# Kernel optimization log

Measured on AMD Instinct MI355X. Metric: run time of the kernel, lower is better.

Reference implementation:

```python
import jax, jax.numpy as jnp
import numpy as np
from jax import lax

E, C, N = 3, 2, 2048          # edge types, channels, nodes (= nb_items)
B, T = 64, 50                 # batch, max_seq_length
W_IN = 256; W_OUT = 256; U = 512  # gcn in/out, rnn_units


def setup_inputs() -> dict:
    key = jax.random.key(0)
    ks = jax.random.split(key, 16)
    # sparse-ish adjacency stored densely (coalesce/spspmm equivalents are dense ops)
    A = jnp.where(jax.random.uniform(ks[0], (E, N, N)) < 0.01,
                  jax.random.uniform(ks[1], (E, N, N)), 0.0)
    X = jax.random.normal(ks[2], (N, W_IN)) * 0.1
    seqs = (jax.random.uniform(ks[3], (B, T, N)) < 0.005).astype(jnp.float32)  # multi-hot baskets
    seq_len = jax.random.randint(ks[4], (B,), 1, T + 1)
    h0 = jnp.zeros((B, U), jnp.float32)
    c0 = jnp.zeros((B, U), jnp.float32)
    # GTConv weights: init constant 1 (softmax -> uniform filter)
    gt_w1 = jnp.ones((C, E), jnp.float32)
    gt_w2 = jnp.ones((C, E), jnp.float32)
    gt_w3 = jnp.ones((C, E), jnp.float32)
    s_in = 1.0 / np.sqrt(W_IN)
    gcn_W = jax.random.normal(ks[5], (W_IN, W_OUT)) * s_in
    gcn_b = jnp.zeros((W_OUT,), jnp.float32)
    lin1_W = jax.random.normal(ks[6], (C * W_OUT, W_OUT)) * (1.0 / np.sqrt(C * W_OUT))
    lin1_b = jnp.zeros((W_OUT,), jnp.float32)
    s_u = 1.0 / np.sqrt(U)
    lstm_Wih = jax.random.normal(ks[7], (4 * U, W_OUT)) * s_u
    lstm_Whh = jax.random.normal(ks[8], (4 * U, U)) * s_u
    lstm_bih = jnp.zeros((4 * U,), jnp.float32)
    lstm_bhh = jnp.zeros((4 * U,), jnp.float32)
    score_W = jax.random.normal(ks[9], (N, U)) * s_u
    return {"A": A, "X": X, "seqs": seqs, "seq_len": seq_len, "h0": h0, "c0": c0,
            "gt_w1": gt_w1, "gt_w2": gt_w2, "gt_w3": gt_w3,
            "gcn_W": gcn_W, "gcn_b": gcn_b, "lin1_W": lin1_W, "lin1_b": lin1_b,
            "lstm_Wih": lstm_Wih, "lstm_Whh": lstm_Whh,
            "lstm_bih": lstm_bih, "lstm_bhh": lstm_bhh, "score_W": score_W}


def _gtconv(A, w):
    # filter = softmax over edge types; per-channel convex combine of adjacencies
    f = jax.nn.softmax(w, axis=1)            # [C,E]
    return jnp.einsum('ce,enm->cnm', f, A)   # [C,N,N]


def _col_normalize(H):
    # remove self loops; deg = scatter_add over col; value *= deg_col^-1 (no_grad deg)
    H = H * (1.0 - jnp.eye(N, dtype=H.dtype))
    deg = H.sum(axis=1)                      # [C,N] per-column degree
    dinv = lax.stop_gradient(jnp.where(deg > 0, 1.0 / deg, 0.0))
    return H * dinv[:, None, :]


def _gcn(M, X, W, b):
    # PyG GCNConv: add self loops, sym-normalize by col/row degree, aggregate at target
    M1 = M + jnp.eye(N, dtype=M.dtype)
    deg = M1.sum(axis=0)                     # scatter over col
    dis = jnp.where(deg > 0, lax.rsqrt(deg), 0.0)
    Ahat = dis[:, None] * M1 * dis[None, :]
    return Ahat.T @ (X @ W) + b              # out[target] = sum_src norm * x[src]


def reference(A, X, seqs, seq_len, h0, c0, gt_w1, gt_w2, gt_w3,
              gcn_W, gcn_b, lin1_W, lin1_b,
              lstm_Wih, lstm_Whh, lstm_bih, lstm_bhh, score_W):
    # --- GT layers: H = conv1(A) @ conv2(A), then H = norm(H) @ conv(A) ---
    HA = _gtconv(A, gt_w1)
    HB = _gtconv(A, gt_w2)
    H = jnp.einsum('cnk,ckm->cnm', HA, HB)          # spspmm per channel
    Hn = _col_normalize(H)
    HB2 = _gtconv(A, gt_w3)
    H = jnp.einsum('cnk,ckm->cnm', Hn, HB2)
    # --- GCN per channel, relu, concat, linear1 ---
    feats = [jax.nn.relu(_gcn(H[i], X, gcn_W, gcn_b)) for i in range(C)]
    X_ = jnp.concatenate(feats, axis=1) @ lin1_W + lin1_b   # [N, W_OUT]
    # --- basket max-pooling over items in each basket (empty -> zeros) ---
    def pool_step(_, mask_t):                # mask_t: [B,N]
        masked = jnp.where(mask_t[:, :, None] > 0, X_[None, :, :], -jnp.inf)
        pooled = masked.max(axis=1)          # [B, W_OUT]
        has = mask_t.sum(axis=1) > 0
        return None, jnp.where(has[:, None], pooled, 0.0)
    _, bs = lax.scan(pool_step, None, jnp.swapaxes(seqs, 0, 1))  # [T,B,W_OUT]
    # --- single-layer LSTM (PyTorch gate order i,f,g,o) ---
    def lstm_step(carry, x_t):
        h, c = carry
        g = x_t @ lstm_Wih.T + h @ lstm_Whh.T + lstm_bih + lstm_bhh
        i, f, gg, o = jnp.split(g, 4, axis=-1)
        c = jax.nn.sigmoid(f) * c + jax.nn.sigmoid(i) * jnp.tanh(gg)
        h = jax.nn.sigmoid(o) * jnp.tanh(c)
        return (h, c), h
    _, outs = lax.scan(lstm_step, (h0, c0), bs)      # [T,B,U]
    lstm_out = jnp.swapaxes(outs, 0, 1)              # [B,T,U]
    actual = lstm_out[jnp.arange(B), seq_len - 1]    # [B,U] last valid step
    return jax.nn.sigmoid(actual @ score_W.T)        # [B,N]
```

## Files before the change

kernel.cpp:

```cpp
#include <hip/hip_runtime.h>
#include <stdint.h>

#define E_ 3
#define C_ 2
#define N_ 2048
#define B_ 64
#define T_ 50
#define WIN_ 256
#define WOUT_ 256
#define U_ 512
#define BT_ (B_*T_)
#define BTP_ 3328

typedef unsigned short u16;
typedef unsigned int u32;
typedef __bf16 bf16x8 __attribute__((ext_vector_type(8)));
typedef float f32x4 __attribute__((ext_vector_type(4)));

#define NN_ (2048LL*2048LL)

__device__ __forceinline__ float bf2f(u16 u){
  u32 x = ((u32)u) << 16; return __builtin_bit_cast(float, x);
}
__device__ __forceinline__ u16 f2bf(float f){
  u32 x = __builtin_bit_cast(u32, f);
  u32 r = (x + 0x7fffu + ((x >> 16) & 1u)) >> 16;
  return (u16)r;
}

__device__ __forceinline__ void gload16(const u16* g, u16* l){
  __builtin_amdgcn_global_load_lds((const __attribute__((address_space(1))) u32*)g,
                                   (__attribute__((address_space(3))) u32*)l, 16, 0, 0);
}

__global__ void k_prep0(const float* __restrict__ w1, const float* __restrict__ w2,
                        const float* __restrict__ w3, float* __restrict__ filt,
                        const float* __restrict__ bih, const float* __restrict__ bhh,
                        float* __restrict__ bsum, u32* __restrict__ flagv,
                        const float* __restrict__ X, u16* __restrict__ Xbf,
                        const float* __restrict__ Wih, u16* __restrict__ Wihbf,
                        const float* __restrict__ scoreW, u16* __restrict__ sWbf){
  const long bx = blockIdx.x;
  if(bx < 8192){
    const long i = bx*256 + threadIdx.x;
    if(i < (long)N_*WIN_) Xbf[i] = f2bf(X[i]);
    else if(i < (long)N_*WIN_ + 4*U_*WOUT_){
      const long j = i - (long)N_*WIN_; Wihbf[j] = f2bf(Wih[j]);
    } else {
      const long j = i - (long)N_*WIN_ - 4*U_*WOUT_; sWbf[j] = f2bf(scoreW[j]);
    }
    return;
  }
  const int i = (int)(bx - 8192)*256 + threadIdx.x;
  bsum[i] = bih[i] + bhh[i];
  flagv[i] = 0;
  if(i < 3*C_){
    const int fi = i / C_, c = i % C_;
    const float* w = (fi==0) ? w1 : ((fi==1) ? w2 : w3);
    float v[E_]; float mx = -3.4e38f;
    for(int e=0;e<E_;e++){ v[e] = w[c*E_+e]; mx = fmaxf(mx, v[e]); }
    float s = 0.f;
    for(int e=0;e<E_;e++){ v[e] = expf(v[e]-mx); s += v[e]; }
    for(int e=0;e<E_;e++) filt[(fi*C_+c)*E_ + e] = v[e]/s;
  }
}

__global__ void k_combineAll3(const float* __restrict__ A, const float* __restrict__ filt,
                              u16* __restrict__ HA, u16* __restrict__ HBt,
                              u16* __restrict__ HB2t){
  __shared__ float te[3][32][33];
  const int ti = blockIdx.x, tj = blockIdx.y;
  const int x = threadIdx.x, y0 = threadIdx.y;
  #pragma unroll
  for(int i=0;i<4;i++){
    const int y = y0 + i*8;
    const long base = (long)(tj*32+y)*N_ + ti*32 + x;
    const float a0 = A[0*NN_+base], a1 = A[1*NN_+base], a2 = A[2*NN_+base];
    te[0][y][x]=a0; te[1][y][x]=a1; te[2][y][x]=a2;
    #pragma unroll
    for(int c=0;c<C_;c++)
      HA[c*NN_ + base] = f2bf(filt[c*E_]*a0 + filt[c*E_+1]*a1 + filt[c*E_+2]*a2);
  }
  __syncthreads();
  #pragma unroll
  for(int i=0;i<4;i++){
    const int y = y0 + i*8;
    const long ob = (long)(ti*32+y)*N_ + tj*32 + x;
    const float a0=te[0][x][y], a1=te[1][x][y], a2=te[2][x][y];
    #pragma unroll
    for(int c=0;c<C_;c++){
      HBt[c*NN_+ob]  = f2bf(filt[(C_+c)*E_]*a0   + filt[(C_+c)*E_+1]*a1   + filt[(C_+c)*E_+2]*a2);
      HB2t[c*NN_+ob] = f2bf(filt[(2*C_+c)*E_]*a0 + filt[(2*C_+c)*E_+1]*a1 + filt[(2*C_+c)*E_+2]*a2);
    }
  }
}

template<int MODE>
__global__ __launch_bounds__(256) void gemm_bt(
    const u16* __restrict__ Ag, const u16* __restrict__ Bg, void* __restrict__ Cg,
    int K, int ldc, long sA, long sB, long sC,
    const float* __restrict__ disv, int sDis, const float* __restrict__ bias)
{
  __shared__ u16 At[2][128*64];
  __shared__ u16 Bt[2][128*64];
  const int tid = threadIdx.x;
  const int w = tid >> 6, l = tid & 63;
  const int z = blockIdx.z;
  const int zc = (MODE==7) ? (z >> 2) : z;
  const int kBase = (MODE==7) ? ((z & 3)*sDis) : 0;
  const u16* Ab = Ag + (long)zc*sA;
  const u16* Bb = Bg + (long)z*sB;
  const int rowBase = blockIdx.y*128;
  const int colBase = blockIdx.x*128;

  f32x4 acc[4][4];
  #pragma unroll
  for(int i=0;i<4;i++)
    #pragma unroll
    for(int j=0;j<4;j++)
      acc[i][j] = f32x4{0.f,0.f,0.f,0.f};

  const int wr = w >> 1, wc = w & 1;
  const int srow = l >> 3;
  const int scol = ((l & 7) ^ srow) << 3;
  const int frow = l & 15;
  const int fkc = l >> 4;

  const int nk = (MODE==7) ? (sDis >> 6) : (K >> 6);
  #pragma unroll
  for(int r=0;r<4;r++){
    const int ch = w*4 + r;
    gload16(Ab + (long)(rowBase + ch*8 + srow)*K + kBase + scol, &At[0][ch*512]);
    gload16(Bb + (long)(colBase + ch*8 + srow)*K + kBase + scol, &Bt[0][ch*512]);
  }
  __syncthreads();

  for(int kt=0; kt<nk; ++kt){
    const int cur = kt & 1;
    if(kt+1 < nk){
      const int k0 = kBase + ((kt+1) << 6);
      #pragma unroll
      for(int r=0;r<4;r++){
        const int ch = w*4 + r;
        gload16(Ab + (long)(rowBase + ch*8 + srow)*K + k0 + scol, &At[cur^1][ch*512]);
        gload16(Bb + (long)(colBase + ch*8 + srow)*K + k0 + scol, &Bt[cur^1][ch*512]);
      }
    }
    #pragma unroll
    for(int ks=0; ks<2; ++ks){
      bf16x8 af[4], bfv[4];
      #pragma unroll
      for(int m=0;m<4;m++){
        const int rr = wr*64 + m*16 + frow;
        af[m] = *(const bf16x8*)&At[cur][rr*64 + (((ks*4 + fkc) ^ (rr&7))<<3)];
      }
      #pragma unroll
      for(int n=0;n<4;n++){
        const int rr = wc*64 + n*16 + frow;
        bfv[n] = *(const bf16x8*)&Bt[cur][rr*64 + (((ks*4 + fkc) ^ (rr&7))<<3)];
      }
      #pragma unroll
      for(int m=0;m<4;m++)
        #pragma unroll
        for(int n=0;n<4;n++)
          acc[m][n] = __builtin_amdgcn_mfma_f32_16x16x32_bf16(af[m], bfv[n], acc[m][n], 0, 0, 0);
    }
    if(kt+1 < nk) __syncthreads();
  }

  #pragma unroll
  for(int m=0;m<4;m++){
    const int row0 = rowBase + wr*64 + m*16 + (l>>4)*4;
    #pragma unroll
    for(int n=0;n<4;n++){
      const int col = colBase + wc*64 + n*16 + (l&15);
      #pragma unroll
      for(int r=0;r<4;r++){
        const float v = acc[m][n][r];
        if(MODE==1){
          ((u16*)Cg)[z*sC + (long)(row0+r)*ldc + col] = f2bf(v);
        } else if(MODE==2){
          float o = disv[z*(long)sDis + row0 + r]*v + bias[col];
          o = o > 0.f ? o : 0.f;
          ((u16*)Cg)[z*sC + (long)(row0+r)*ldc + col] = f2bf(o);
        } else if(MODE==3){
          ((float*)Cg)[z*sC + (long)(row0+r)*ldc + col] = v + bias[col];
        } else if(MODE==4){
          const int row = row0 + r;
          if(row < BT_){
            const int bb = row/50, tt = row - bb*50;
            const int gate = col >> 9, ugg = col & 511;
            ((float*)Cg)[((((long)tt*4 + (bb>>4))*512 + ugg)*16 + (bb&15))*4 + gate] = v + bias[col];
          }
        } else if(MODE==5){
          const int row = row0 + r;
          const float o = (v + (row==col ? 1.f : 0.f)) * disv[z*(long)sDis + col];
          ((u16*)Cg)[z*sC + (long)row*ldc + col] = f2bf(o);
        } else if(MODE==6){
          const int row = row0 + r;
          if(row < B_)
            ((float*)Cg)[(long)row*ldc + col] = 1.f/(1.f + expf(-v));
        } else if(MODE==7){
          ((float*)Cg)[((long)z*N_ + row0 + r)*WOUT_ + col] = v;
        }
      }
    }
  }
}

__global__ void k_catred(const float* __restrict__ P, const float* __restrict__ disv,
                         const float* __restrict__ gcnB, u16* __restrict__ catb){
  const int idx = blockIdx.x*256 + threadIdx.x;
  const int row = idx >> 9;
  const int cf  = idx & 511;
  const int c = cf >> 8, f = cf & 255;
  float s = 0.f;
  #pragma unroll
  for(int ks=0;ks<4;ks++)
    s += P[(((long)(c*4+ks)*N_ + row)<<8) + f];
  float o = disv[c*N_ + row]*s + gcnB[f];
  catb[(long)row*(C_*WOUT_) + cf] = f2bf(o > 0.f ? o : 0.f);
}

__global__ void k_degpart(const u16* __restrict__ H, float* __restrict__ partial){
  const int c = blockIdx.z;
  const int col = blockIdx.x*256 + threadIdx.x;
  const int r0 = blockIdx.y*128;
  const u16* Hc = H + c*NN_;
  float s = 0.f;
  #pragma unroll 4
  for(int r=0;r<128;r++) s += bf2f(Hc[(long)(r0+r)*N_ + col]);
  partial[((long)c*16 + blockIdx.y)*N_ + col] = s;
}

__global__ void k_dinv(const u16* __restrict__ H, const float* __restrict__ partial,
                       float* __restrict__ dinvb){
  const int i = blockIdx.x*256 + threadIdx.x;
  const int c = i >> 11, m = i & (N_-1);
  float s = 0.f;
  #pragma unroll
  for(int p=0;p<16;p++) s += partial[((long)c*16 + p)*N_ + m];
  s -= bf2f(H[c*NN_ + (long)m*N_ + m]);
  dinvb[i] = s > 0.f ? 1.f/s : 0.f;
}

__global__ void k_colscale_dis(u16* __restrict__ H, const float* __restrict__ dinvb,
                               const u16* __restrict__ HB2t, float* __restrict__ disv){
  const int c = blockIdx.y;
  if(blockIdx.x < 16384){
    const long i = (long)blockIdx.x*256 + threadIdx.x;
    const int j = (int)(i >> 11), ii = (int)(i & (N_-1));
    const long idx = c*NN_ + i;
    const float v = (j==ii) ? 0.f : bf2f(H[idx])*dinvb[c*N_ + ii];
    H[idx] = f2bf(v);
    return;
  }
  const int j = blockIdx.x - 16384;
  const u16* r = HB2t + (c*(long)N_ + j)*N_;
  const float* dv = dinvb + c*N_;
  float s = 0.f;
  for(int i=threadIdx.x;i<N_;i+=256)
    if(dv[i] > 0.f) s += bf2f(r[i]);
  __shared__ float red[256];
  red[threadIdx.x] = s;
  __syncthreads();
  for(int st=128; st>0; st>>=1){
    if(threadIdx.x < st) red[threadIdx.x] += red[threadIdx.x+st];
    __syncthreads();
  }
  if(threadIdx.x==0){
    const float deg = red[0] + 1.f;
    disv[c*N_ + j] = deg > 0.f ? rsqrtf(deg) : 0.f;
  }
}

__global__ void k_transpose3(const float* __restrict__ gcnW, u16* __restrict__ Wt,
                             const float* __restrict__ lin1W, u16* __restrict__ l1Wt){
  const float* in; u16* out; int R, Cc;
  if(blockIdx.z==0){ in=gcnW;  out=Wt;   R=WIN_;     Cc=WOUT_; }
  else { in=lin1W; out=l1Wt; R=C_*WOUT_; Cc=WOUT_; }
  const int ti = blockIdx.x, tj = blockIdx.y;
  if(ti >= (Cc>>5) || tj >= (R>>5)) return;
  __shared__ float tt[32][33];
  const int x = threadIdx.x, y0 = threadIdx.y;
  #pragma unroll
  for(int i=0;i<4;i++){
    const int y = y0 + i*8;
    tt[y][x] = in[(long)(tj*32+y)*Cc + ti*32 + x];
  }
  __syncthreads();
  #pragma unroll
  for(int i=0;i<4;i++){
    const int y = y0 + i*8;
    out[(long)(ti*32+y)*R + tj*32 + x] = f2bf(tt[x][y]);
  }
}

__global__ void k_pool(const float* __restrict__ seqs, const float* __restrict__ X_,
                       u16* __restrict__ bs){
  const int t = blockIdx.x, b = blockIdx.y;
  const int f = threadIdx.x;
  if(t >= T_){
    bs[(long)(BT_ + b*2 + (t-T_))*WOUT_ + f] = 0;
    return;
  }
  const float* mask = seqs + ((long)b*T_ + t)*N_;
  __shared__ int list[N_];
  __shared__ int cnt;
  if(f==0) cnt = 0;
  __syncthreads();
  {
    const float4 m0 = *(const float4*)&mask[f*8];
    const float4 m1 = *(const float4*)&mask[f*8+4];
    const float mv[8] = {m0.x,m0.y,m0.z,m0.w,m1.x,m1.y,m1.z,m1.w};
    #pragma unroll
    for(int q=0;q<8;q++){
      if(mv[q] > 0.f){
        int p = atomicAdd(&cnt, 1);
        list[p] = f*8 + q;
      }
    }
  }
  __syncthreads();
  const int m = cnt;
  float mx = -3.4e38f;
  for(int i=0;i<m;i++)
    mx = fmaxf(mx, X_[(long)list[i]*WOUT_ + f]);
  bs[((long)b*T_ + t)*WOUT_ + f] = f2bf(m>0 ? mx : 0.f);
}

__global__ void k_packWhh3(const float* __restrict__ Whh, u16* __restrict__ P,
                           const float* __restrict__ h0, u16* __restrict__ Hglob){
  const long idx = (long)blockIdx.x*256 + threadIdx.x;
  const int e  = (int)(idx & 7);
  const int kk = (int)((idx >> 3) & 15);
  const int l  = (int)((idx >> 7) & 63);
  const int w  = (int)((idx >> 13) & 7);
  const int s  = (int)(idx >> 16);
  const int lr = w*16 + (l & 15);
  const int gam = lr & 3, ui = lr >> 2;
  const int grow = gam*512 + s*32 + ui;
  const int k = kk*32 + (l >> 4)*8 + e;
  P[idx] = f2bf(Whh[(long)grow*512 + k]);
  if(idx < 32768){
    const int b = (int)(idx >> 9), u = (int)(idx & 511);
    const int grp = b >> 4, bl = b & 15;
    Hglob[grp*16384 + (bl << 9) + (u ^ ((bl & 7) << 3))] = f2bf(h0[idx]);
  }
}

__global__ __launch_bounds__(512) void k_lstm_all(
    const u16* __restrict__ WhhP, const float* __restrict__ Gq,
    const float* __restrict__ c0v, const int* __restrict__ seqlen,
    u16* __restrict__ Hglob, u32* __restrict__ flagv, u16* __restrict__ act)
{
  __shared__ u16 Hl[16*512];
  const int tid = threadIdx.x;
  const int w = tid >> 6, l = tid & 63;
  const int grp = blockIdx.x & 3, s = blockIdx.x >> 2;
  const int fr = l & 15, hi = l >> 4;

  bf16x8 wreg[16];
  const u16* wp = WhhP + (((long)s*8 + w)*64 + l)*128;
  #pragma unroll
  for(int kk=0; kk<16; ++kk)
    wreg[kk] = *(const bf16x8*)&wp[kk*8];

  const int ug = s*32 + w*4 + hi;
  const int bl = fr;
  const int bg = grp*16 + bl;
  float cst = c0v[bg*U_ + ug];
  const int sl = seqlen[bg] - 1;
  u16* Hbase = Hglob + grp*16384;
  const int hswz = (bl & 7) << 3;
  const int fi = (grp*16 + fr)*32;
  const long gqbase = (((long)grp*512 + ug)*16 + bl)*4;
  float4 gq_nxt = *(const float4*)&Gq[gqbase];

  for(int t=0; t<T_; ++t){
    const float4 gq = gq_nxt;
    const u16* Hin = Hbase + (t & 1)*8192;
    #pragma unroll
    for(int r=0; r<2; ++r)
      gload16(Hin + (r*8 + w)*512 + l*8, &Hl[(r*8 + w)*512]);
    __syncthreads();

    f32x4 acc = f32x4{0.f,0.f,0.f,0.f};
    #pragma unroll
    for(int kk=0; kk<16; ++kk){
      const int ke = kk*32 + hi*8;
      bf16x8 bb = *(const bf16x8*)&Hl[(bl << 9) + (ke ^ hswz)];
      acc = __builtin_amdgcn_mfma_f32_16x16x32_bf16(wreg[kk], bb, acc, 0, 0, 0);
    }

    if(t+1 < T_)
      gq_nxt = *(const float4*)&Gq[(long)(t+1)*(4*2048*16) + gqbase];

    const float a0 = acc[0] + gq.x;
    const float a1 = acc[1] + gq.y;
    const float a2 = acc[2] + gq.z;
    const float a3 = acc[3] + gq.w;
    const float ig = 1.f/(1.f + expf(-a0));
    const float fg = 1.f/(1.f + expf(-a1));
    const float gg = tanhf(a2);
    const float og = 1.f/(1.f + expf(-a3));
    cst = fg*cst + ig*gg;
    const float h = og*tanhf(cst);
    u16* Hout = Hbase + ((t+1) & 1)*8192;
    Hout[(bl << 9) + (ug ^ hswz)] = f2bf(h);
    if(sl == t) act[bg*U_ + ug] = f2bf(h);

    if(t == T_-1) break;
    __syncthreads();
    if(tid == 0)
      __hip_atomic_store(&flagv[(grp*16 + s)*32], (u32)(t+1),
                         __ATOMIC_RELEASE, __HIP_MEMORY_SCOPE_AGENT);
    if(w == 0){
      while(__hip_atomic_load(&flagv[fi], __ATOMIC_ACQUIRE,
                              __HIP_MEMORY_SCOPE_AGENT) <= (u32)t){
        __builtin_amdgcn_s_sleep(1);
      }
    }
    __syncthreads();
  }
}

extern "C" void kernel_launch(void* const* d_in, const int* in_sizes, int n_in,
                              void* d_out, int out_size, void* d_ws, size_t ws_size,
                              hipStream_t stream){
  (void)in_sizes; (void)n_in; (void)out_size; (void)ws_size;
  const float* A      = (const float*)d_in[0];
  const float* X      = (const float*)d_in[1];
  const float* seqs   = (const float*)d_in[2];
  const int*   seqlen = (const int*)d_in[3];
  const float* h0     = (const float*)d_in[4];
  const float* c0     = (const float*)d_in[5];
  const float* gtw1   = (const float*)d_in[6];
  const float* gtw2   = (const float*)d_in[7];
  const float* gtw3   = (const float*)d_in[8];
  const float* gcnW   = (const float*)d_in[9];
  const float* gcnB   = (const float*)d_in[10];
  const float* lin1W  = (const float*)d_in[11];
  const float* lin1B  = (const float*)d_in[12];
  const float* Wih    = (const float*)d_in[13];
  const float* Whh    = (const float*)d_in[14];
  const float* bihp   = (const float*)d_in[15];
  const float* bhhp   = (const float*)d_in[16];
  const float* scoreW = (const float*)d_in[17];

  char* ws = (char*)d_ws;
  u16* buf0 = (u16*)(ws + 0);
  u16* buf1 = (u16*)(ws + 16777216);
  u16* buf2 = (u16*)(ws + 33554432);
  char* S0  = ws + 50331648;
  float* filt  = (float*)(S0 + 0);
  float* disv  = (float*)(S0 + 1024);
  u16*  Wt     = (u16*) (S0 + 17408);
  u16*  XWt    = (u16*) (S0 + 148480);
  u16*  catb   = (u16*) (S0 + 1197056);
  u16*  l1Wt   = (u16*) (S0 + 3294208);
  float* Xo    = (float*)(S0 + 3556352);
  u16*  bs     = (u16*) (S0 + 5653504);
  u16*  act    = (u16*) (S0 + 7357440);
  u16*  sWbf   = (u16*) (S0 + 7488512);
  u16*  WhhB   = (u16*) (S0 + 9585664);
  u16*  Xbf    = (u16*) (S0 + 11682816);
  u16*  Wihbf  = (u16*) (S0 + 12731392);
  float* bsum  = (float*)(S0 + 13779968);
  u16*  Hglob  = (u16*) (S0 + 13788160);
  u32*  flagv  = (u32*) (S0 + 13919232);
  float* degp  = (float*)(S0 + 14050304);
  float* dinvb = (float*)(S0 + 14312448);
  u16* buf3 = (u16*)(ws + 64660480);
  u16* HA   = buf0;
  u16* HBt  = buf1;
  u16* Hb   = buf2;
  u16* HB2t = buf3;
  u16* Pd   = buf1;
  float* Pcat = (float*)ws;
  float* Gq = (float*)ws;

  k_prep0<<<dim3(8200), 256, 0, stream>>>(gtw1, gtw2, gtw3, filt, bihp, bhhp, bsum, flagv,
                                          X, Xbf, Wih, Wihbf, scoreW, sWbf);
  k_combineAll3<<<dim3(N_/32, N_/32), dim3(32,8), 0, stream>>>(A, filt, HA, HBt, HB2t);
  k_transpose3<<<dim3(16, 64, 2), dim3(32,8), 0, stream>>>(gcnW, Wt, lin1W, l1Wt);
  gemm_bt<1><<<dim3(16,16,C_), 256, 0, stream>>>(HA, HBt, Hb, N_, N_, NN_, NN_, NN_, nullptr, 0, nullptr);
  k_degpart<<<dim3(8, 16, C_), 256, 0, stream>>>(Hb, degp);
  k_dinv<<<dim3(16), 256, 0, stream>>>(Hb, degp, dinvb);
  k_colscale_dis<<<dim3(16384 + N_, C_), 256, 0, stream>>>(Hb, dinvb, HB2t, disv);
  gemm_bt<5><<<dim3(16,16,C_), 256, 0, stream>>>(HB2t, Hb, Pd, N_, N_, NN_, NN_, NN_, disv, N_, nullptr);
  gemm_bt<1><<<dim3(N_/128, WOUT_/128, 1), 256, 0, stream>>>(Wt, Xbf, XWt, WIN_, N_, 0, 0, 0, nullptr, 0, nullptr);
  gemm_bt<7><<<dim3(WOUT_/128, N_/128, C_*4), 256, 0, stream>>>(Pd, XWt, Pcat, N_, 0, NN_, 0, 0, nullptr, 512, nullptr);
  k_catred<<<dim3(4096), 256, 0, stream>>>(Pcat, disv, gcnB, catb);
  gemm_bt<3><<<dim3(WOUT_/128, N_/128, 1), 256, 0, stream>>>(catb, l1Wt, Xo, C_*WOUT_, WOUT_, 0, 0, 0, nullptr, 0, lin1B);
  k_pool<<<dim3(52, B_), 256, 0, stream>>>(seqs, Xo, bs);
  gemm_bt<4><<<dim3((4*U_)/128, BTP_/128, 1), 256, 0, stream>>>(bs, Wihbf, Gq, WOUT_, 0, 0, 0, 0, nullptr, 0, bsum);
  k_packWhh3<<<dim3(4096), 256, 0, stream>>>(Whh, WhhB, h0, Hglob);
  k_lstm_all<<<dim3(64), 512, 0, stream>>>(WhhB, Gq, c0, seqlen, Hglob, flagv, act);
  gemm_bt<6><<<dim3(N_/128, 1, 1), 256, 0, stream>>>(act, sWbf, (float*)d_out, U_, N_, 0, 0, 0, nullptr, 0, nullptr);
}
```

Baseline: 484.9 us.

## Repartition LSTM into 8 batch groups, fold transposes into prep, swizzle GEMM tiles

```diff
diff --git a/kernel.cpp b/kernel.cpp
--- a/kernel.cpp
+++ b/kernel.cpp
@@ -39,10 +39,14 @@
                         float* __restrict__ bsum, u32* __restrict__ flagv,
                         const float* __restrict__ X, u16* __restrict__ Xbf,
                         const float* __restrict__ Wih, u16* __restrict__ Wihbf,
-                        const float* __restrict__ scoreW, u16* __restrict__ sWbf){
+                        const float* __restrict__ scoreW, u16* __restrict__ sWbf,
+                        const float* __restrict__ gcnW, u16* __restrict__ Wt,
+                        const float* __restrict__ lin1W, u16* __restrict__ l1Wt){
+  __shared__ float tt[32][33];
   const long bx = blockIdx.x;
+  const int tid = threadIdx.x;
   if(bx < 8192){
-    const long i = bx*256 + threadIdx.x;
+    const long i = bx*256 + tid;
     if(i < (long)N_*WIN_) Xbf[i] = f2bf(X[i]);
     else if(i < (long)N_*WIN_ + 4*U_*WOUT_){
       const long j = i - (long)N_*WIN_; Wihbf[j] = f2bf(Wih[j]);
@@ -51,17 +55,36 @@
     }
     return;
   }
-  const int i = (int)(bx - 8192)*256 + threadIdx.x;
-  bsum[i] = bih[i] + bhh[i];
-  flagv[i] = 0;
-  if(i < 3*C_){
-    const int fi = i / C_, c = i % C_;
-    const float* w = (fi==0) ? w1 : ((fi==1) ? w2 : w3);
-    float v[E_]; float mx = -3.4e38f;
-    for(int e=0;e<E_;e++){ v[e] = w[c*E_+e]; mx = fmaxf(mx, v[e]); }
-    float s = 0.f;
-    for(int e=0;e<E_;e++){ v[e] = expf(v[e]-mx); s += v[e]; }
-    for(int e=0;e<E_;e++) filt[(fi*C_+c)*E_ + e] = v[e]/s;
+  if(bx < 8200){
+    const int i = (int)(bx - 8192)*256 + tid;
+    bsum[i] = bih[i] + bhh[i];
+    flagv[i] = 0;
+    if(i < 3*C_){
+      const int fi = i / C_, c = i % C_;
+      const float* w = (fi==0) ? w1 : ((fi==1) ? w2 : w3);
+      float v[E_]; float mx = -3.4e38f;
+      for(int e=0;e<E_;e++){ v[e] = w[c*E_+e]; mx = fmaxf(mx, v[e]); }
+      float s = 0.f;
+      for(int e=0;e<E_;e++){ v[e] = expf(v[e]-mx); s += v[e]; }
+      for(int e=0;e<E_;e++) filt[(fi*C_+c)*E_ + e] = v[e]/s;
+    }
+    return;
+  }
+  int r = (int)(bx - 8200);
+  const float* in; u16* out; int R, Cc, ti, tj;
+  if(r < 64){ in=gcnW; out=Wt; R=WIN_; Cc=WOUT_; ti=r&7; tj=r>>3; }
+  else { r -= 64; in=lin1W; out=l1Wt; R=C_*WOUT_; Cc=WOUT_; ti=r&7; tj=r>>3; }
+  const int x = tid & 31, y0 = tid >> 5;
+  #pragma unroll
+  for(int i=0;i<4;i++){
+    const int y = y0 + i*8;
+    tt[y][x] = in[(long)(tj*32+y)*Cc + ti*32 + x];
+  }
+  __syncthreads();
+  #pragma unroll
+  for(int i=0;i<4;i++){
+    const int y = y0 + i*8;
+    out[(long)(ti*32+y)*R + tj*32 + x] = f2bf(tt[x][y]);
   }
 }
 
@@ -106,12 +129,18 @@
   const int tid = threadIdx.x;
   const int w = tid >> 6, l = tid & 63;
   const int z = blockIdx.z;
+  int bxi = blockIdx.x, byi = blockIdx.y;
+  if((MODE==1 || MODE==5) && gridDim.y == 16){
+    const int lin = byi*16 + bxi;
+    const int t2 = (lin & 7)*32 + (lin >> 3);
+    bxi = t2 & 15; byi = t2 >> 4;
+  }
   const int zc = (MODE==7) ? (z >> 2) : z;
   const int kBase = (MODE==7) ? ((z & 3)*sDis) : 0;
   const u16* Ab = Ag + (long)zc*sA;
   const u16* Bb = Bg + (long)z*sB;
-  const int rowBase = blockIdx.y*128;
-  const int colBase = blockIdx.x*128;
+  const int rowBase = byi*128;
+  const int colBase = bxi*128;
 
   f32x4 acc[4][4];
   #pragma unroll
@@ -190,7 +219,7 @@
           if(row < BT_){
             const int bb = row/50, tt = row - bb*50;
             const int gate = col >> 9, ugg = col & 511;
-            ((float*)Cg)[((((long)tt*4 + (bb>>4))*512 + ugg)*16 + (bb&15))*4 + gate] = v + bias[col];
+            ((float*)Cg)[((((long)tt*8 + (bb>>3))*512 + ugg)*8 + (bb&7))*4 + gate] = v + bias[col];
           }
         } else if(MODE==5){
           const int row = row0 + r;
@@ -274,28 +303,6 @@
   }
 }
 
-__global__ void k_transpose3(const float* __restrict__ gcnW, u16* __restrict__ Wt,
-                             const float* __restrict__ lin1W, u16* __restrict__ l1Wt){
-  const float* in; u16* out; int R, Cc;
-  if(blockIdx.z==0){ in=gcnW;  out=Wt;   R=WIN_;     Cc=WOUT_; }
-  else { in=lin1W; out=l1Wt; R=C_*WOUT_; Cc=WOUT_; }
-  const int ti = blockIdx.x, tj = blockIdx.y;
-  if(ti >= (Cc>>5) || tj >= (R>>5)) return;
-  __shared__ float tt[32][33];
-  const int x = threadIdx.x, y0 = threadIdx.y;
-  #pragma unroll
-  for(int i=0;i<4;i++){
-    const int y = y0 + i*8;
-    tt[y][x] = in[(long)(tj*32+y)*Cc + ti*32 + x];
-  }
-  __syncthreads();
-  #pragma unroll
-  for(int i=0;i<4;i++){
-    const int y = y0 + i*8;
-    out[(long)(ti*32+y)*R + tj*32 + x] = f2bf(tt[x][y]);
-  }
-}
-
 __global__ void k_pool(const float* __restrict__ seqs, const float* __restrict__ X_,
                        u16* __restrict__ bs){
   const int t = blockIdx.x, b = blockIdx.y;
@@ -329,23 +336,24 @@
   bs[((long)b*T_ + t)*WOUT_ + f] = f2bf(m>0 ? mx : 0.f);
 }
 
-__global__ void k_packWhh3(const float* __restrict__ Whh, u16* __restrict__ P,
+__global__ void k_packWhh4(const float* __restrict__ Whh, u16* __restrict__ P,
                            const float* __restrict__ h0, u16* __restrict__ Hglob){
   const long idx = (long)blockIdx.x*256 + threadIdx.x;
   const int e  = (int)(idx & 7);
   const int kk = (int)((idx >> 3) & 15);
-  const int l  = (int)((idx >> 7) & 63);
-  const int w  = (int)((idx >> 13) & 7);
-  const int s  = (int)(idx >> 16);
-  const int lr = w*16 + (l & 15);
-  const int gam = lr & 3, ui = lr >> 2;
-  const int grow = gam*512 + s*32 + ui;
+  const int rf = (int)((idx >> 7) & 1);
+  const int l  = (int)((idx >> 8) & 63);
+  const int w  = (int)((idx >> 14) & 7);
+  const int s  = (int)(idx >> 17);
+  const int fr16 = l & 15;
+  const int gate = fr16 & 3, u4 = fr16 >> 2;
+  const int grow = gate*512 + s*64 + w*8 + rf*4 + u4;
   const int k = kk*32 + (l >> 4)*8 + e;
   P[idx] = f2bf(Whh[(long)grow*512 + k]);
   if(idx < 32768){
     const int b = (int)(idx >> 9), u = (int)(idx & 511);
-    const int grp = b >> 4, bl = b & 15;
-    Hglob[grp*16384 + (bl << 9) + (u ^ ((bl & 7) << 3))] = f2bf(h0[idx]);
+    const int grp = b >> 3, bl = b & 7;
+    Hglob[grp*8192 + (bl << 9) + (u ^ (bl << 3))] = f2bf(h0[idx]);
   }
 }
 
@@ -354,66 +362,84 @@
     const float* __restrict__ c0v, const int* __restrict__ seqlen,
     u16* __restrict__ Hglob, u32* __restrict__ flagv, u16* __restrict__ act)
 {
-  __shared__ u16 Hl[16*512];
+  __shared__ u16 Hl[2*8*512];
   const int tid = threadIdx.x;
   const int w = tid >> 6, l = tid & 63;
-  const int grp = blockIdx.x & 3, s = blockIdx.x >> 2;
-  const int fr = l & 15, hi = l >> 4;
-
-  bf16x8 wreg[16];
-  const u16* wp = WhhP + (((long)s*8 + w)*64 + l)*128;
-  #pragma unroll
-  for(int kk=0; kk<16; ++kk)
-    wreg[kk] = *(const bf16x8*)&wp[kk*8];
-
-  const int ug = s*32 + w*4 + hi;
-  const int bl = fr;
-  const int bg = grp*16 + bl;
-  float cst = c0v[bg*U_ + ug];
-  const int sl = seqlen[bg] - 1;
-  u16* Hbase = Hglob + grp*16384;
-  const int hswz = (bl & 7) << 3;
-  const int fi = (grp*16 + fr)*32;
-  const long gqbase = (((long)grp*512 + ug)*16 + bl)*4;
-  float4 gq_nxt = *(const float4*)&Gq[gqbase];
+  const int grp = blockIdx.x & 7, s = blockIdx.x >> 3;
+  const int hi = l >> 4;
+
+  bf16x8 wreg[32];
+  const u16* wp = WhhP + (((long)s*8 + w)*64 + l)*256;
+  #pragma unroll
+  for(int i=0;i<32;++i) wreg[i] = *(const bf16x8*)&wp[i*8];
+
+  const int bl = l & 15;
+  const bool valid = bl < 8;
+  const int blr = bl & 7;
+  const int bg = grp*8 + blr;
+  const int ug0 = s*64 + w*8 + hi;
+  float cst0 = 0.f, cst1 = 0.f;
+  int sl = -2;
+  if(valid){
+    cst0 = c0v[bg*U_ + ug0];
+    cst1 = c0v[bg*U_ + ug0 + 4];
+    sl = seqlen[bg] - 1;
+  }
+  u16* Hbase = Hglob + grp*8192;
+  const int rsw = blr << 3;
+  const int fi = (grp*8 + (l & 7))*32;
+  const long gq0 = (((long)grp*512 + ug0)*8 + blr)*4;
+  float4 gqn0 = *(const float4*)&Gq[gq0];
+  float4 gqn1 = *(const float4*)&Gq[gq0 + 128];
 
   for(int t=0; t<T_; ++t){
-    const float4 gq = gq_nxt;
-    const u16* Hin = Hbase + (t & 1)*8192;
-    #pragma unroll
-    for(int r=0; r<2; ++r)
-      gload16(Hin + (r*8 + w)*512 + l*8, &Hl[(r*8 + w)*512]);
+    const float4 gqa = gqn0, gqb = gqn1;
+    const u16* Hin = Hbase + (t & 1)*4096;
+    gload16(Hin + w*512 + l*8, &Hl[(t & 1)*4096 + w*512]);
     __syncthreads();
 
-    f32x4 acc = f32x4{0.f,0.f,0.f,0.f};
+    f32x4 acc0 = f32x4{0.f,0.f,0.f,0.f};
+    f32x4 acc1 = f32x4{0.f,0.f,0.f,0.f};
+    const u16* Hb_ = &Hl[(t & 1)*4096 + (blr << 9)];
     #pragma unroll
     for(int kk=0; kk<16; ++kk){
       const int ke = kk*32 + hi*8;
-      bf16x8 bb = *(const bf16x8*)&Hl[(bl << 9) + (ke ^ hswz)];
-      acc = __builtin_amdgcn_mfma_f32_16x16x32_bf16(wreg[kk], bb, acc, 0, 0, 0);
-    }
-
-    if(t+1 < T_)
-      gq_nxt = *(const float4*)&Gq[(long)(t+1)*(4*2048*16) + gqbase];
-
-    const float a0 = acc[0] + gq.x;
-    const float a1 = acc[1] + gq.y;
-    const float a2 = acc[2] + gq.z;
-    const float a3 = acc[3] + gq.w;
-    const float ig = 1.f/(1.f + expf(-a0));
-    const float fg = 1.f/(1.f + expf(-a1));
-    const float gg = tanhf(a2);
-    const float og = 1.f/(1.f + expf(-a3));
-    cst = fg*cst + ig*gg;
-    const float h = og*tanhf(cst);
-    u16* Hout = Hbase + ((t+1) & 1)*8192;
-    Hout[(bl << 9) + (ug ^ hswz)] = f2bf(h);
-    if(sl == t) act[bg*U_ + ug] = f2bf(h);
+      bf16x8 bb = *(const bf16x8*)&Hb_[ke ^ rsw];
+      acc0 = __builtin_amdgcn_mfma_f32_16x16x32_bf16(wreg[kk],    bb, acc0, 0, 0, 0);
+      acc1 = __builtin_amdgcn_mfma_f32_16x16x32_bf16(wreg[16+kk], bb, acc1, 0, 0, 0);
+    }
+
+    if(t+1 < T_){
+      gqn0 = *(const float4*)&Gq[(long)(t+1)*131072 + gq0];
+      gqn1 = *(const float4*)&Gq[(long)(t+1)*131072 + gq0 + 128];
+    }
+
+    u16* Hout = Hbase + ((t+1) & 1)*4096;
+    if(valid){
+      {
+        const float a0=acc0[0]+gqa.x, a1=acc0[1]+gqa.y, a2=acc0[2]+gqa.z, a3=acc0[3]+gqa.w;
+        const float ig=1.f/(1.f+expf(-a0)), fg=1.f/(1.f+expf(-a1));
+        const float gg=tanhf(a2), og=1.f/(1.f+expf(-a3));
+        cst0 = fg*cst0 + ig*gg;
+        const float h = og*tanhf(cst0);
+        Hout[(blr << 9) + (ug0 ^ rsw)] = f2bf(h);
+        if(sl==t) act[bg*U_ + ug0] = f2bf(h);
+      }
+      {
+        const float a0=acc1[0]+gqb.x, a1=acc1[1]+gqb.y, a2=acc1[2]+gqb.z, a3=acc1[3]+gqb.w;
+        const float ig=1.f/(1.f+expf(-a0)), fg=1.f/(1.f+expf(-a1));
+        const float gg=tanhf(a2), og=1.f/(1.f+expf(-a3));
+        cst1 = fg*cst1 + ig*gg;
+        const float h = og*tanhf(cst1);
+        Hout[(blr << 9) + ((ug0+4) ^ rsw)] = f2bf(h);
+        if(sl==t) act[bg*U_ + ug0 + 4] = f2bf(h);
+      }
+    }
 
     if(t == T_-1) break;
     __syncthreads();
     if(tid == 0)
-      __hip_atomic_store(&flagv[(grp*16 + s)*32], (u32)(t+1),
+      __hip_atomic_store(&flagv[(grp*8 + s)*32], (u32)(t+1),
                          __ATOMIC_RELEASE, __HIP_MEMORY_SCOPE_AGENT);
     if(w == 0){
       while(__hip_atomic_load(&flagv[fi], __ATOMIC_ACQUIRE,
@@ -480,10 +506,10 @@
   float* Pcat = (float*)ws;
   float* Gq = (float*)ws;
 
-  k_prep0<<<dim3(8200), 256, 0, stream>>>(gtw1, gtw2, gtw3, filt, bihp, bhhp, bsum, flagv,
-                                          X, Xbf, Wih, Wihbf, scoreW, sWbf);
+  k_prep0<<<dim3(8392), 256, 0, stream>>>(gtw1, gtw2, gtw3, filt, bihp, bhhp, bsum, flagv,
+                                          X, Xbf, Wih, Wihbf, scoreW, sWbf,
+                                          gcnW, Wt, lin1W, l1Wt);
   k_combineAll3<<<dim3(N_/32, N_/32), dim3(32,8), 0, stream>>>(A, filt, HA, HBt, HB2t);
-  k_transpose3<<<dim3(16, 64, 2), dim3(32,8), 0, stream>>>(gcnW, Wt, lin1W, l1Wt);
   gemm_bt<1><<<dim3(16,16,C_), 256, 0, stream>>>(HA, HBt, Hb, N_, N_, NN_, NN_, NN_, nullptr, 0, nullptr);
   k_degpart<<<dim3(8, 16, C_), 256, 0, stream>>>(Hb, degp);
   k_dinv<<<dim3(16), 256, 0, stream>>>(Hb, degp, dinvb);
@@ -495,7 +521,7 @@
   gemm_bt<3><<<dim3(WOUT_/128, N_/128, 1), 256, 0, stream>>>(catb, l1Wt, Xo, C_*WOUT_, WOUT_, 0, 0, 0, nullptr, 0, lin1B);
   k_pool<<<dim3(52, B_), 256, 0, stream>>>(seqs, Xo, bs);
   gemm_bt<4><<<dim3((4*U_)/128, BTP_/128, 1), 256, 0, stream>>>(bs, Wihbf, Gq, WOUT_, 0, 0, 0, 0, nullptr, 0, bsum);
-  k_packWhh3<<<dim3(4096), 256, 0, stream>>>(Whh, WhhB, h0, Hglob);
+  k_packWhh4<<<dim3(4096), 256, 0, stream>>>(Whh, WhhB, h0, Hglob);
   k_lstm_all<<<dim3(64), 512, 0, stream>>>(WhhB, Gq, c0, seqlen, Hglob, flagv, act);
   gemm_bt<6><<<dim3(N_/128, 1, 1), 256, 0, stream>>>(act, sWbf, (float*)d_out, U_, N_, 0, 0, 0, nullptr, 0, nullptr);
 }
```

New measurement: 486.3 us. About the same (+0.3%).
